# Performance work log

Hardware: AMD Instinct MI355X
Metric: run time of the kernel (lower is better)

## Reference

```python
import jax, jax.numpy as jnp
import numpy as np

B, N, H = 32, 1024, 256
ALPHA = 0.2  # leaky relu slope
NEG_INF = -1e12


def setup_inputs() -> dict:
    key = jax.random.key(0)
    k1, k2, k3, k4, k5, k6 = jax.random.split(key, 6)
    inp = jax.random.normal(k1, (B, N, H), dtype=jnp.float32)
    A = (jax.random.uniform(k2, (B, N, N)) < 0.05).astype(jnp.float32)
    l = jnp.sort(jax.random.randint(k3, (B, 2), 0, N), axis=1)
    # xavier-uniform(gain=1.414) approximated; exact init values are irrelevant for correctness
    lim_w = 1.414 * np.sqrt(6.0 / (H + H))
    W_i = jax.random.uniform(k4, (H, H), minval=-lim_w, maxval=lim_w, dtype=jnp.float32)
    W_c = jax.random.uniform(k5, (H, H), minval=-lim_w, maxval=lim_w, dtype=jnp.float32)
    lim_a = 1.414 * np.sqrt(6.0 / (2 * H + 1))
    a = jax.random.uniform(k6, (2 * H, 1), minval=-lim_a, maxval=lim_a, dtype=jnp.float32)
    return {"inp": inp, "A": A, "l": l, "W_i": W_i, "W_c": W_c, "a": a}


def reference(inp, A, l, W_i, W_c, a):
    # eval mode: dropout is identity (training=False)
    n = inp.shape[1]
    h = inp.shape[2]
    Wh_i = jnp.einsum('bnh,he->bne', inp, W_i)
    Wh_c = jnp.einsum('bnh,he->bne', inp, W_c)
    # vectorized replacement of the per-batch Wh[index][i:j] = Wh_i[index][i:j] loop
    idx = jnp.arange(n)
    sel = (idx[None, :] >= l[:, 0:1]) & (idx[None, :] < l[:, 1:2])  # [B,N]
    Wh = jnp.where(sel[:, :, None], Wh_i, Wh_c)
    # additive attention scores
    Wh1 = Wh @ a[:h, :]  # [B,N,1]
    Wh2 = Wh @ a[h:, :]  # [B,N,1]
    A_ = A + jnp.eye(n, dtype=A.dtype)
    e = jax.nn.leaky_relu((Wh1 + jnp.swapaxes(Wh2, 1, 2)) * A_, ALPHA)
    att = jnp.where(A_ > 0, e, NEG_INF)
    att = jax.nn.softmax(att, axis=2)
    h_prime = jnp.einsum('bnm,bme->bne', att, Wh)
    return jax.nn.elu(h_prime)  # concat=True
```

## Files before the change

### kernel.cpp

```cpp
#include <hip/hip_runtime.h>
#include <hip/hip_bf16.h>
#include <stdint.h>

#define B_ 32
#define N_ 1024
#define H_ 256
#define PF_PITCH 520

typedef short bf16x8 __attribute__((ext_vector_type(8)));
typedef float floatx4 __attribute__((ext_vector_type(4)));

__device__ inline unsigned short f2bs(float x) {
    __hip_bfloat16 h = __float2bfloat16(x);
    return __builtin_bit_cast(unsigned short, h);
}

__global__ __launch_bounds__(256)
void k_uvec(const float* __restrict__ Wi, const float* __restrict__ Wc,
            const float* __restrict__ a, float* __restrict__ U) {
    int k = blockIdx.x;
    int t = threadIdx.x;
    float wi = Wi[k * H_ + t];
    float wc = Wc[k * H_ + t];
    float a1 = a[t], a2 = a[H_ + t];
    float p0 = wi * a1, p1 = wc * a1, p2 = wi * a2, p3 = wc * a2;
    for (int off = 32; off; off >>= 1) {
        p0 += __shfl_xor(p0, off);
        p1 += __shfl_xor(p1, off);
        p2 += __shfl_xor(p2, off);
        p3 += __shfl_xor(p3, off);
    }
    __shared__ float red[4][4];
    int w = t >> 6;
    if ((t & 63) == 0) { red[w][0] = p0; red[w][1] = p1; red[w][2] = p2; red[w][3] = p3; }
    __syncthreads();
    if (t == 0) {
        U[0 * H_ + k] = red[0][0] + red[1][0] + red[2][0] + red[3][0];
        U[1 * H_ + k] = red[0][1] + red[1][1] + red[2][1] + red[3][1];
        U[2 * H_ + k] = red[0][2] + red[1][2] + red[2][2] + red[3][2];
        U[3 * H_ + k] = red[0][3] + red[1][3] + red[2][3] + red[3][3];
    }
}

__global__ __launch_bounds__(256)
void k_prep(const float* __restrict__ Wi, const float* __restrict__ Wc,
            unsigned short* __restrict__ WtFi, unsigned short* __restrict__ WtFc) {
    __shared__ float tile[64][65];
    int mat = blockIdx.x >> 4;
    int tr = ((blockIdx.x >> 2) & 3) * 64;
    int tc = (blockIdx.x & 3) * 64;
    const float* W = mat ? Wc : Wi;
    unsigned short* WtF = mat ? WtFc : WtFi;
    int t = threadIdx.x;
    int rr = t >> 2, c4 = (t & 3) * 16;
    const float* src = W + (size_t)(tr + rr) * H_ + tc + c4;
#pragma unroll
    for (int j = 0; j < 4; ++j) {
        float4 v = *reinterpret_cast<const float4*>(src + j * 4);
        tile[rr][c4 + 4 * j + 0] = v.x;
        tile[rr][c4 + 4 * j + 1] = v.y;
        tile[rr][c4 + 4 * j + 2] = v.z;
        tile[rr][c4 + 4 * j + 3] = v.w;
    }
    __syncthreads();
#pragma unroll
    for (int h = 0; h < 2; ++h) {
        int s = h * 256 + t;
        int ksl = s >> 8;
        int cl  = (s >> 6) & 3;
        int ll  = s & 63;
        int m16v = ll & 15, quadv = ll >> 4;
        int nloc = cl * 16 + m16v;
        int kb = ksl * 32 + quadv * 8;
        unsigned int pk[4];
#pragma unroll
        for (int jj = 0; jj < 4; ++jj) {
            unsigned short lo = f2bs(tile[kb + 2 * jj][nloc]);
            unsigned short hi = f2bs(tile[kb + 2 * jj + 1][nloc]);
            pk[jj] = (unsigned int)lo | ((unsigned int)hi << 16);
        }
        int ksg = (tr >> 5) + ksl;
        int cg  = (tc >> 4) + cl;
        *reinterpret_cast<uint4*>(WtF + ((size_t)(ksg * 16 + cg) * 64 + ll) * 8) =
            *reinterpret_cast<uint4*>(pk);
    }
}

__global__ __launch_bounds__(256)
void k_gemm(const float* __restrict__ inp, const int* __restrict__ l,
            const unsigned short* __restrict__ WtFi, const unsigned short* __restrict__ WtFc,
            unsigned short* __restrict__ WhF, const float* __restrict__ U,
            float* __restrict__ Wh1, float* __restrict__ Wh2) {
    __shared__ unsigned short bbuf[2][4096];
    int blk = blockIdx.x;
    int b  = blk >> 5;
    int r0 = ((blk >> 1) & 15) * 64;
    int n0 = (blk & 1) * 128;
    int t = threadIdx.x;
    int w = t >> 6;
    int lane = t & 63;
    int quad = lane >> 4, m16 = lane & 15;
    int rowb = r0 + w * 16;

    int l0 = l[2 * b], l1 = l[2 * b + 1];
    bool allI = (l0 <= r0) && (r0 + 64 <= l1);
    bool allC = (l1 <= r0) || (l0 >= r0 + 64);
    int npass = (allI || allC) ? 1 : 2;

    int row = rowb + m16;
    bool sel = (row >= l0) && (row < l1);
    const float* xrow = inp + ((size_t)(b * N_ + row)) * H_;
    const float* u1 = U + (sel ? 0 : H_);
    const float* u2 = U + 2 * H_ + (sel ? 0 : H_);
    bool doWh = (n0 == 0);
    float d1 = 0.f, d2 = 0.f;

    unsigned short* fb = WhF + (size_t)b * (N_ * H_);
    int cb = n0 >> 4;

    int j0 = rowb + quad * 4;
    int ksO = j0 >> 5;
    int laneF = m16 + 16 * ((j0 & 31) >> 3);
    int jj0 = j0 & 7;

    for (int pass = 0; pass < npass; ++pass) {
        const unsigned short* WtF =
            (npass == 1) ? (allI ? WtFi : WtFc) : (pass == 0 ? WtFi : WtFc);
        const unsigned short* gbase = WtF + cb * 512;

        floatx4 acc[8];
#pragma unroll
        for (int c = 0; c < 8; ++c) acc[c] = (floatx4){0.f, 0.f, 0.f, 0.f};

        {
            uint4 v0 = *reinterpret_cast<const uint4*>(gbase + (size_t)t * 8);
            uint4 v1 = *reinterpret_cast<const uint4*>(gbase + (size_t)(256 + t) * 8);
            *reinterpret_cast<uint4*>(&bbuf[0][t * 8]) = v0;
            *reinterpret_cast<uint4*>(&bbuf[0][(256 + t) * 8]) = v1;
        }
        for (int ks = 0; ks < 8; ++ks) {
            __syncthreads();
            uint4 v0, v1;
            if (ks < 7) {
                v0 = *reinterpret_cast<const uint4*>(gbase + (size_t)(ks + 1) * 8192 + t * 8);
                v1 = *reinterpret_cast<const uint4*>(gbase + (size_t)(ks + 1) * 8192 + (256 + t) * 8);
            }
            const float4 xa = *reinterpret_cast<const float4*>(xrow + ks * 32 + quad * 8);
            const float4 xb = *reinterpret_cast<const float4*>(xrow + ks * 32 + quad * 8 + 4);
            if (pass == 0 && doWh) {
                const float4 ua = *reinterpret_cast<const float4*>(u1 + ks * 32 + quad * 8);
                const float4 ub = *reinterpret_cast<const float4*>(u1 + ks * 32 + quad * 8 + 4);
                const float4 va = *reinterpret_cast<const float4*>(u2 + ks * 32 + quad * 8);
                const float4 vb = *reinterpret_cast<const float4*>(u2 + ks * 32 + quad * 8 + 4);
                d1 += xa.x * ua.x + xa.y * ua.y + xa.z * ua.z + xa.w * ua.w
                    + xb.x * ub.x + xb.y * ub.y + xb.z * ub.z + xb.w * ub.w;
                d2 += xa.x * va.x + xa.y * va.y + xa.z * va.z + xa.w * va.w
                    + xb.x * vb.x + xb.y * vb.y + xb.z * vb.z + xb.w * vb.w;
            }
            unsigned int pk0 = (unsigned int)f2bs(xa.x) | ((unsigned int)f2bs(xa.y) << 16);
            unsigned int pk1 = (unsigned int)f2bs(xa.z) | ((unsigned int)f2bs(xa.w) << 16);
            unsigned int pk2 = (unsigned int)f2bs(xb.x) | ((unsigned int)f2bs(xb.y) << 16);
            unsigned int pk3 = (unsigned int)f2bs(xb.z) | ((unsigned int)f2bs(xb.w) << 16);
            uint4 apk = {pk0, pk1, pk2, pk3};
            bf16x8 af = __builtin_bit_cast(bf16x8, apk);

            const unsigned short* bptr = &bbuf[ks & 1][lane * 8];
#pragma unroll
            for (int c = 0; c < 8; ++c) {
                bf16x8 bfr = *reinterpret_cast<const bf16x8*>(bptr + c * 512);
                acc[c] = __builtin_amdgcn_mfma_f32_16x16x32_bf16(af, bfr, acc[c], 0, 0, 0);
            }
            if (ks < 7) {
                *reinterpret_cast<uint4*>(&bbuf[(ks + 1) & 1][t * 8]) = v0;
                *reinterpret_cast<uint4*>(&bbuf[(ks + 1) & 1][(256 + t) * 8]) = v1;
            }
        }
        __syncthreads();

#pragma unroll
        for (int c = 0; c < 8; ++c) {
            size_t base = ((size_t)((ksO * 16 + cb + c) * 64) + laneF) * 8 + jj0;
            if (npass == 1) {
                unsigned int lo = (unsigned int)f2bs(acc[c][0]) | ((unsigned int)f2bs(acc[c][1]) << 16);
                unsigned int hi = (unsigned int)f2bs(acc[c][2]) | ((unsigned int)f2bs(acc[c][3]) << 16);
                uint2 v = {lo, hi};
                *reinterpret_cast<uint2*>(fb + base) = v;
            } else {
                bool want[4]; bool all = true, none = true;
#pragma unroll
                for (int r = 0; r < 4; ++r) {
                    int j = j0 + r;
                    bool s2 = (j >= l0) && (j < l1);
                    want[r] = (pass == 0) ? s2 : !s2;
                    all = all && want[r]; none = none && !want[r];
                }
                if (all) {
                    unsigned int lo = (unsigned int)f2bs(acc[c][0]) | ((unsigned int)f2bs(acc[c][1]) << 16);
                    unsigned int hi = (unsigned int)f2bs(acc[c][2]) | ((unsigned int)f2bs(acc[c][3]) << 16);
                    uint2 v = {lo, hi};
                    *reinterpret_cast<uint2*>(fb + base) = v;
                } else if (!none) {
#pragma unroll
                    for (int r = 0; r < 4; ++r)
                        if (want[r]) fb[base + r] = f2bs(acc[c][r]);
                }
            }
        }
    }

    if (doWh) {
        d1 += __shfl_xor(d1, 16); d1 += __shfl_xor(d1, 32);
        d2 += __shfl_xor(d2, 16); d2 += __shfl_xor(d2, 32);
        if (quad == 0) {
            Wh1[b * N_ + rowb + m16] = d1;
            Wh2[b * N_ + rowb + m16] = d2;
        }
    }
}

__global__ __launch_bounds__(256)
void k_attn(const float* __restrict__ A, const float* __restrict__ Wh1,
            const float* __restrict__ Wh2, const unsigned short* __restrict__ WhF,
            float* __restrict__ out) {
    __shared__ unsigned short pfrag[2][32 * PF_PITCH];
    int t = threadIdx.x, w = t >> 6, lane = t & 63;
    int bi = blockIdx.x;
    int b = (bi & 7) * 4 + (bi >> 8);
    int tile = (bi >> 3) & 31;
    int rowbase = tile * 32;

    const float* Wh2b = Wh2 + b * N_;
    float4 w2v[4];
#pragma unroll
    for (int ch = 0; ch < 4; ++ch)
        w2v[ch] = *reinterpret_cast<const float4*>(Wh2b + ch * 256 + lane * 4);

    int ksl = lane >> 3;
    int q2 = (lane >> 1) & 3;
    int jj0 = (lane & 1) * 4;

#pragma unroll
    for (int tt = 0; tt < 2; ++tt) {
#pragma unroll
        for (int q = 0; q < 4; ++q) {
            int m = w * 4 + q;
            int i = rowbase + tt * 16 + m;
            float wh1 = Wh1[b * N_ + i];
            const float* Arow = A + ((size_t)(b * N_ + i)) * N_;
            int s = m + 16 * q2;
            int sw = s ^ ((s >> 3) & 7);
            int sls = sw * 8 + jj0;
#pragma unroll
            for (int ch = 0; ch < 4; ++ch) {
                float4 av = *reinterpret_cast<const float4*>(Arow + ch * 256 + lane * 4);
                if ((i >> 2) == (ch * 64 + lane)) ((float*)&av)[i & 3] += 1.0f;
                float aa[4] = {av.x, av.y, av.z, av.w};
                float ww[4] = {w2v[ch].x, w2v[ch].y, w2v[ch].z, w2v[ch].w};
                float p[4];
#pragma unroll
                for (int c = 0; c < 4; ++c) {
                    float e  = (wh1 + ww[c]) * aa[c];
                    float lv = fmaxf(e, 0.2f * e);
                    p[c] = aa[c] > 0.f ? __expf(lv) : 0.f;
                }
                unsigned int lo = (unsigned int)f2bs(p[0]) | ((unsigned int)f2bs(p[1]) << 16);
                unsigned int hi = (unsigned int)f2bs(p[2]) | ((unsigned int)f2bs(p[3]) << 16);
                uint2 v = {lo, hi};
                int ks = ch * 8 + ksl;
                *reinterpret_cast<uint2*>(pfrag[tt] + ks * PF_PITCH + sls) = v;
            }
        }
    }
    __syncthreads();

    const unsigned short* WB = WhF + (size_t)b * (N_ * H_);
    int rs = (lane ^ ((lane >> 3) & 7)) * 8;
    unsigned short oneb = f2bs(1.0f);
    bf16x8 bones = {(short)oneb, (short)oneb, (short)oneb, (short)oneb,
                    (short)oneb, (short)oneb, (short)oneb, (short)oneb};
    floatx4 acc0[4], acc1[4], sum0, sum1;
    sum0 = (floatx4){0.f, 0.f, 0.f, 0.f};
    sum1 = (floatx4){0.f, 0.f, 0.f, 0.f};
#pragma unroll
    for (int cc = 0; cc < 4; ++cc) {
        acc0[cc] = (floatx4){0.f, 0.f, 0.f, 0.f};
        acc1[cc] = (floatx4){0.f, 0.f, 0.f, 0.f};
    }
#pragma unroll 2
    for (int ks = 0; ks < 32; ++ks) {
        bf16x8 af0 = *reinterpret_cast<const bf16x8*>(pfrag[0] + ks * PF_PITCH + rs);
        bf16x8 af1 = *reinterpret_cast<const bf16x8*>(pfrag[1] + ks * PF_PITCH + rs);
        sum0 = __builtin_amdgcn_mfma_f32_16x16x32_bf16(af0, bones, sum0, 0, 0, 0);
        sum1 = __builtin_amdgcn_mfma_f32_16x16x32_bf16(af1, bones, sum1, 0, 0, 0);
#pragma unroll
        for (int cc = 0; cc < 4; ++cc) {
            int c = w * 4 + cc;
            bf16x8 bfv = *reinterpret_cast<const bf16x8*>(
                WB + ((size_t)((ks * 16 + c) * 64 + lane)) * 8);
            acc0[cc] = __builtin_amdgcn_mfma_f32_16x16x32_bf16(af0, bfv, acc0[cc], 0, 0, 0);
            acc1[cc] = __builtin_amdgcn_mfma_f32_16x16x32_bf16(af1, bfv, acc1[cc], 0, 0, 0);
        }
    }

    int quad = lane >> 4, m16 = lane & 15;
    float inv0[4], inv1[4];
#pragma unroll
    for (int r = 0; r < 4; ++r) {
        inv0[r] = 1.0f / sum0[r];
        inv1[r] = 1.0f / sum1[r];
    }
#pragma unroll
    for (int cc = 0; cc < 4; ++cc) {
        int col = (w * 4 + cc) * 16 + m16;
#pragma unroll
        for (int r = 0; r < 4; ++r) {
            int m = quad * 4 + r;
            float v0 = acc0[cc][r] * inv0[r];
            v0 = v0 > 0.f ? v0 : __expf(v0) - 1.0f;
            out[((size_t)(b * N_ + rowbase + m)) * H_ + col] = v0;
            float v1 = acc1[cc][r] * inv1[r];
            v1 = v1 > 0.f ? v1 : __expf(v1) - 1.0f;
            out[((size_t)(b * N_ + rowbase + 16 + m)) * H_ + col] = v1;
        }
    }
}

extern "C" void kernel_launch(void* const* d_in, const int* in_sizes, int n_in,
                              void* d_out, int out_size, void* d_ws, size_t ws_size,
                              hipStream_t stream) {
    const float* inp = (const float*)d_in[0];
    const float* A   = (const float*)d_in[1];
    const int*   l   = (const int*)d_in[2];
    const float* Wi  = (const float*)d_in[3];
    const float* Wc  = (const float*)d_in[4];
    const float* a   = (const float*)d_in[5];
    float* out = (float*)d_out;

    char* ws = (char*)d_ws;
    size_t off = 0;
    unsigned short* WhF  = (unsigned short*)(ws + off); off += (size_t)B_ * N_ * H_ * 2;
    float* Wh1 = (float*)(ws + off); off += (size_t)B_ * N_ * 4;
    float* Wh2 = (float*)(ws + off); off += (size_t)B_ * N_ * 4;
    float* U   = (float*)(ws + off); off += 4 * H_ * 4;
    unsigned short* WtFi = (unsigned short*)(ws + off); off += (size_t)H_ * H_ * 2;
    unsigned short* WtFc = (unsigned short*)(ws + off); off += (size_t)H_ * H_ * 2;

    k_uvec<<<H_, 256, 0, stream>>>(Wi, Wc, a, U);
    k_prep<<<32, 256, 0, stream>>>(Wi, Wc, WtFi, WtFc);
    k_gemm<<<B_ * 16 * 2, 256, 0, stream>>>(inp, l, WtFi, WtFc, WhF, U, Wh1, Wh2);
    k_attn<<<B_ * (N_ / 32), 256, 0, stream>>>(A, Wh1, Wh2, WhF, out);
}
```

Before: 282.4 us.

## Process attention row tiles sequentially with single LDS buffer and batched A loads

```diff
diff --git a/kernel.cpp b/kernel.cpp
--- a/kernel.cpp
+++ b/kernel.cpp
@@ -218,43 +218,61 @@
     }
 }
 
-__global__ __launch_bounds__(256)
+__global__ __launch_bounds__(256, 4)
 void k_attn(const float* __restrict__ A, const float* __restrict__ Wh1,
             const float* __restrict__ Wh2, const unsigned short* __restrict__ WhF,
             float* __restrict__ out) {
-    __shared__ unsigned short pfrag[2][32 * PF_PITCH];
+    __shared__ unsigned short pfrag[32 * PF_PITCH];
     int t = threadIdx.x, w = t >> 6, lane = t & 63;
     int bi = blockIdx.x;
     int b = (bi & 7) * 4 + (bi >> 8);
     int tile = (bi >> 3) & 31;
     int rowbase = tile * 32;
 
-    const float* Wh2b = Wh2 + b * N_;
-    float4 w2v[4];
-#pragma unroll
-    for (int ch = 0; ch < 4; ++ch)
-        w2v[ch] = *reinterpret_cast<const float4*>(Wh2b + ch * 256 + lane * 4);
-
     int ksl = lane >> 3;
     int q2 = (lane >> 1) & 3;
     int jj0 = (lane & 1) * 4;
 
-#pragma unroll
+    const unsigned short* WB = WhF + (size_t)b * (N_ * H_);
+    int rs = (lane ^ ((lane >> 3) & 7)) * 8;
+    unsigned short oneb = f2bs(1.0f);
+    bf16x8 bones = {(short)oneb, (short)oneb, (short)oneb, (short)oneb,
+                    (short)oneb, (short)oneb, (short)oneb, (short)oneb};
+    int quad = lane >> 4, m16 = lane & 15;
+
     for (int tt = 0; tt < 2; ++tt) {
+        if (tt) __syncthreads();
+
+        const float* Wh2b = Wh2 + b * N_;
+        float4 w2v[4];
+#pragma unroll
+        for (int ch = 0; ch < 4; ++ch)
+            w2v[ch] = *reinterpret_cast<const float4*>(Wh2b + ch * 256 + lane * 4);
+
+        float4 av[4][4];
+        float wh1v[4];
+#pragma unroll
+        for (int q = 0; q < 4; ++q) {
+            int i = rowbase + tt * 16 + w * 4 + q;
+            wh1v[q] = Wh1[b * N_ + i];
+            const float* Arow = A + ((size_t)(b * N_ + i)) * N_;
+#pragma unroll
+            for (int ch = 0; ch < 4; ++ch)
+                av[q][ch] = *reinterpret_cast<const float4*>(Arow + ch * 256 + lane * 4);
+        }
 #pragma unroll
         for (int q = 0; q < 4; ++q) {
             int m = w * 4 + q;
             int i = rowbase + tt * 16 + m;
-            float wh1 = Wh1[b * N_ + i];
-            const float* Arow = A + ((size_t)(b * N_ + i)) * N_;
+            float wh1 = wh1v[q];
             int s = m + 16 * q2;
             int sw = s ^ ((s >> 3) & 7);
             int sls = sw * 8 + jj0;
 #pragma unroll
             for (int ch = 0; ch < 4; ++ch) {
-                float4 av = *reinterpret_cast<const float4*>(Arow + ch * 256 + lane * 4);
-                if ((i >> 2) == (ch * 64 + lane)) ((float*)&av)[i & 3] += 1.0f;
-                float aa[4] = {av.x, av.y, av.z, av.w};
+                float4 avv = av[q][ch];
+                if ((i >> 2) == (ch * 64 + lane)) ((float*)&avv)[i & 3] += 1.0f;
+                float aa[4] = {avv.x, avv.y, avv.z, avv.w};
                 float ww[4] = {w2v[ch].x, w2v[ch].y, w2v[ch].z, w2v[ch].w};
                 float p[4];
 #pragma unroll
@@ -267,60 +285,43 @@
                 unsigned int hi = (unsigned int)f2bs(p[2]) | ((unsigned int)f2bs(p[3]) << 16);
                 uint2 v = {lo, hi};
                 int ks = ch * 8 + ksl;
-                *reinterpret_cast<uint2*>(pfrag[tt] + ks * PF_PITCH + sls) = v;
-            }
-        }
-    }
-    __syncthreads();
-
-    const unsigned short* WB = WhF + (size_t)b * (N_ * H_);
-    int rs = (lane ^ ((lane >> 3) & 7)) * 8;
-    unsigned short oneb = f2bs(1.0f);
-    bf16x8 bones = {(short)oneb, (short)oneb, (short)oneb, (short)oneb,
-                    (short)oneb, (short)oneb, (short)oneb, (short)oneb};
-    floatx4 acc0[4], acc1[4], sum0, sum1;
-    sum0 = (floatx4){0.f, 0.f, 0.f, 0.f};
-    sum1 = (floatx4){0.f, 0.f, 0.f, 0.f};
-#pragma unroll
-    for (int cc = 0; cc < 4; ++cc) {
-        acc0[cc] = (floatx4){0.f, 0.f, 0.f, 0.f};
-        acc1[cc] = (floatx4){0.f, 0.f, 0.f, 0.f};
-    }
+                *reinterpret_cast<uint2*>(pfrag + ks * PF_PITCH + sls) = v;
+            }
+        }
+        __syncthreads();
+
+        floatx4 acc[4], sum;
+        sum = (floatx4){0.f, 0.f, 0.f, 0.f};
+#pragma unroll
+        for (int cc = 0; cc < 4; ++cc)
+            acc[cc] = (floatx4){0.f, 0.f, 0.f, 0.f};
 #pragma unroll 2
-    for (int ks = 0; ks < 32; ++ks) {
-        bf16x8 af0 = *reinterpret_cast<const bf16x8*>(pfrag[0] + ks * PF_PITCH + rs);
-        bf16x8 af1 = *reinterpret_cast<const bf16x8*>(pfrag[1] + ks * PF_PITCH + rs);
-        sum0 = __builtin_amdgcn_mfma_f32_16x16x32_bf16(af0, bones, sum0, 0, 0, 0);
-        sum1 = __builtin_amdgcn_mfma_f32_16x16x32_bf16(af1, bones, sum1, 0, 0, 0);
+        for (int ks = 0; ks < 32; ++ks) {
+            bf16x8 af = *reinterpret_cast<const bf16x8*>(pfrag + ks * PF_PITCH + rs);
+            sum = __builtin_amdgcn_mfma_f32_16x16x32_bf16(af, bones, sum, 0, 0, 0);
+#pragma unroll
+            for (int cc = 0; cc < 4; ++cc) {
+                int c = w * 4 + cc;
+                bf16x8 bfv = *reinterpret_cast<const bf16x8*>(
+                    WB + ((size_t)((ks * 16 + c) * 64 + lane)) * 8);
+                acc[cc] = __builtin_amdgcn_mfma_f32_16x16x32_bf16(af, bfv, acc[cc], 0, 0, 0);
+            }
+        }
+
+        float inv[4];
+#pragma unroll
+        for (int r = 0; r < 4; ++r)
+            inv[r] = 1.0f / sum[r];
 #pragma unroll
         for (int cc = 0; cc < 4; ++cc) {
-            int c = w * 4 + cc;
-            bf16x8 bfv = *reinterpret_cast<const bf16x8*>(
-                WB + ((size_t)((ks * 16 + c) * 64 + lane)) * 8);
-            acc0[cc] = __builtin_amdgcn_mfma_f32_16x16x32_bf16(af0, bfv, acc0[cc], 0, 0, 0);
-            acc1[cc] = __builtin_amdgcn_mfma_f32_16x16x32_bf16(af1, bfv, acc1[cc], 0, 0, 0);
-        }
-    }
-
-    int quad = lane >> 4, m16 = lane & 15;
-    float inv0[4], inv1[4];
-#pragma unroll
-    for (int r = 0; r < 4; ++r) {
-        inv0[r] = 1.0f / sum0[r];
-        inv1[r] = 1.0f / sum1[r];
-    }
-#pragma unroll
-    for (int cc = 0; cc < 4; ++cc) {
-        int col = (w * 4 + cc) * 16 + m16;
-#pragma unroll
-        for (int r = 0; r < 4; ++r) {
-            int m = quad * 4 + r;
-            float v0 = acc0[cc][r] * inv0[r];
-            v0 = v0 > 0.f ? v0 : __expf(v0) - 1.0f;
-            out[((size_t)(b * N_ + rowbase + m)) * H_ + col] = v0;
-            float v1 = acc1[cc][r] * inv1[r];
-            v1 = v1 > 0.f ? v1 : __expf(v1) - 1.0f;
-            out[((size_t)(b * N_ + rowbase + 16 + m)) * H_ + col] = v1;
+            int col = (w * 4 + cc) * 16 + m16;
+#pragma unroll
+            for (int r = 0; r < 4; ++r) {
+                int m = quad * 4 + r;
+                float v0 = acc[cc][r] * inv[r];
+                v0 = v0 > 0.f ? v0 : __expf(v0) - 1.0f;
+                out[((size_t)(b * N_ + rowbase + tt * 16 + m)) * H_ + col] = v0;
+            }
         }
     }
 }
```

New measurement: 287.3 us. No clear change (+1.7%).
